# Kernel tuning notes

Hardware: AMD Instinct MI355X
Metric: run time of the kernel (lower is better)

The kernel has to match this reference:

```python
import jax, jax.numpy as jnp
import numpy as np

B, T, I, H, O = 64, 512, 256, 512, 256


def setup_inputs() -> dict:
    key = jax.random.key(0)
    ks = jax.random.split(key, 11)
    s_in = 1.0 / np.sqrt(H)  # torch nn.RNN init scale ~ U(-1/sqrt(H), 1/sqrt(H))
    return {
        "x": jax.random.normal(ks[0], (B, T, I), jnp.float32),
        "W_ih0": jax.random.normal(ks[1], (H, I), jnp.float32) * s_in,
        "W_hh0": jax.random.normal(ks[2], (H, H), jnp.float32) * s_in,
        "b_ih0": jax.random.normal(ks[3], (H,), jnp.float32) * s_in,
        "b_hh0": jax.random.normal(ks[4], (H,), jnp.float32) * s_in,
        "W_ih1": jax.random.normal(ks[5], (H, H), jnp.float32) * s_in,
        "W_hh1": jax.random.normal(ks[6], (H, H), jnp.float32) * s_in,
        "b_ih1": jax.random.normal(ks[7], (H,), jnp.float32) * s_in,
        "b_hh1": jax.random.normal(ks[8], (H,), jnp.float32) * s_in,
        "W_fc": jax.random.normal(ks[9], (O, H), jnp.float32) * s_in,
        "b_fc": jax.random.normal(ks[10], (O,), jnp.float32) * s_in,
    }


def _rnn_layer(xs, W_ih, W_hh, b_ih, b_hh):
    # xs: [T, B, in]; precompute input projection as one big GEMM
    pre = jnp.einsum("tbi,hi->tbh", xs, W_ih) + b_ih + b_hh  # [T, B, H]

    def step(h, p):
        h = jnp.tanh(p + h @ W_hh.T)
        return h, h

    h0 = jnp.zeros((xs.shape[1], W_hh.shape[0]), xs.dtype)
    h_last, ys = jax.lax.scan(step, h0, pre)
    return ys, h_last  # ys: [T, B, H]


def reference(x, W_ih0, W_hh0, b_ih0, b_hh0, W_ih1, W_hh1, b_ih1, b_hh1, W_fc, b_fc):
    xs = jnp.transpose(x, (1, 0, 2))  # time-major [T, B, I]
    ys0, _ = _rnn_layer(xs, W_ih0, W_hh0, b_ih0, b_hh0)
    _, h_last = _rnn_layer(ys0, W_ih1, W_hh1, b_ih1, b_hh1)
    return h_last @ W_fc.T + b_fc  # [B, O]
```

## Files before the change

kernel.cpp:

```cpp
#include <hip/hip_runtime.h>

#define BB 64
#define TT 512
#define II 256
#define HH 512
#define OO 256

typedef _Float16 f16;
typedef _Float16 half8 __attribute__((ext_vector_type(8)));
typedef _Float16 half4 __attribute__((ext_vector_type(4)));
typedef float f32x4 __attribute__((ext_vector_type(4)));
typedef unsigned long long u64;

#define SENT 0x7C017C017C017C01ull

union U16 { u64 q[2]; half8 h; };

__device__ __forceinline__ u64 llc_load(const f16* p) {
  return __hip_atomic_load((const u64*)p, __ATOMIC_RELAXED, __HIP_MEMORY_SCOPE_SYSTEM);
}
__device__ __forceinline__ void llc_store(f16* p, u64 v) {
  __hip_atomic_store((u64*)p, v, __ATOMIC_RELAXED, __HIP_MEMORY_SCOPE_SYSTEM);
}

__global__ void prep_sent(u64* __restrict__ dst, size_t n) {
  size_t tid = (size_t)blockIdx.x * blockDim.x + threadIdx.x;
  size_t stride = (size_t)gridDim.x * blockDim.x;
  for (size_t i = tid; i < n; i += stride) dst[i] = SENT;
}

__global__ void prep_x(const float* __restrict__ x, f16* __restrict__ xt) {
  size_t tid = (size_t)blockIdx.x * blockDim.x + threadIdx.x;
  size_t stride = (size_t)gridDim.x * blockDim.x;
  size_t nv = (size_t)TT * BB * II / 4;
  for (size_t v = tid; v < nv; v += stride) {
    size_t i = v * 4;
    size_t t = i >> 14;
    size_t rem = i & 16383;
    size_t b = rem >> 8;
    size_t ii = rem & 255;
    float4 f = *(const float4*)(x + b * (size_t)(TT * II) + t * II + ii);
    half4 h;
    h.x = (f16)f.x; h.y = (f16)f.y; h.z = (f16)f.z; h.w = (f16)f.w;
    *(half4*)(xt + i) = h;
  }
}

__global__ void prep_w(const float* __restrict__ wih0, const float* __restrict__ whh0,
                       const float* __restrict__ wih1, const float* __restrict__ whh1,
                       const float* __restrict__ bih0, const float* __restrict__ bhh0,
                       const float* __restrict__ bih1, const float* __restrict__ bhh1,
                       f16* __restrict__ o0, f16* __restrict__ o1,
                       f16* __restrict__ o2, f16* __restrict__ o3,
                       float* __restrict__ bs0, float* __restrict__ bs1) {
  const size_t n0 = (size_t)HH * II, n1 = (size_t)HH * HH;
  const size_t total = n0 + 3 * n1 + 2 * HH;
  size_t stride = (size_t)gridDim.x * blockDim.x;
  for (size_t i = (size_t)blockIdx.x * blockDim.x + threadIdx.x; i < total; i += stride) {
    size_t j = i;
    if (j < n0) { o0[j] = (f16)wih0[j]; continue; } j -= n0;
    if (j < n1) { o1[j] = (f16)whh0[j]; continue; } j -= n1;
    if (j < n1) { o2[j] = (f16)wih1[j]; continue; } j -= n1;
    if (j < n1) { o3[j] = (f16)whh1[j]; continue; } j -= n1;
    if (j < HH) { bs0[j] = bih0[j] + bhh0[j]; continue; } j -= HH;
    bs1[j] = bih1[j] + bhh1[j];
  }
}

__device__ __forceinline__ void load_valid16(const f16* base, u64* q) {
  for (int iter = 0; iter < 400000; ++iter) {
#pragma unroll
    for (int kf = 0; kf < 16; ++kf) {
      q[2 * kf]     = llc_load(base + kf * 32);
      q[2 * kf + 1] = llc_load(base + kf * 32 + 4);
    }
    int ok = 1;
#pragma unroll
    for (int i = 0; i < 32; ++i) ok &= (q[i] != SENT);
    if (__all(ok)) return;
  }
}

__global__ __launch_bounds__(64, 1) void rnn_seq(
    const f16* __restrict__ xt, f16* __restrict__ ys0, f16* __restrict__ h1h,
    const f16* __restrict__ wih0, const f16* __restrict__ whh0,
    const f16* __restrict__ wih1, const f16* __restrict__ whh1,
    const float* __restrict__ bs0, const float* __restrict__ bs1,
    const float* __restrict__ wfc, const float* __restrict__ bfc,
    float* __restrict__ out) {
  const int wg = blockIdx.x;
  const int layer = wg >> 6;
  const int c = (wg >> 4) & 3;
  const int s = wg & 15;
  const int lane = threadIdx.x;
  const int fr = lane & 15;
  const int kg = lane >> 4;
  const int n0 = s * 32;

  __shared__ f16 tile[16 * 32];

  if (layer == 0) {
    half8 wbi[2][8], wbh[2][16];
#pragma unroll
    for (int j = 0; j < 2; ++j) {
      const f16* wi = wih0 + (size_t)(n0 + j * 16 + fr) * II + kg * 8;
#pragma unroll
      for (int kf = 0; kf < 8; ++kf) wbi[j][kf] = *(const half8*)(wi + kf * 32);
      const f16* wh = whh0 + (size_t)(n0 + j * 16 + fr) * HH + kg * 8;
#pragma unroll
      for (int kf = 0; kf < 16; ++kf) wbh[j][kf] = *(const half8*)(wh + kf * 32);
    }
    const float bias[2] = {bs0[n0 + fr], bs0[n0 + 16 + fr]};
    f32x4 pacc[2][2] = {{{0,0,0,0},{0,0,0,0}},{{0,0,0,0},{0,0,0,0}}};
    {
      const f16* xa = xt + ((size_t)0 * BB + c * 16 + fr) * II + kg * 8;
#pragma unroll
      for (int kf = 0; kf < 8; ++kf) {
        half8 a = *(const half8*)(xa + kf * 32);
        pacc[0][kf & 1] = __builtin_amdgcn_mfma_f32_16x16x32_f16(a, wbi[0][kf], pacc[0][kf & 1], 0, 0, 0);
        pacc[1][kf & 1] = __builtin_amdgcn_mfma_f32_16x16x32_f16(a, wbi[1][kf], pacc[1][kf & 1], 0, 0, 0);
      }
    }
    for (int t = 0; t < TT; ++t) {
      f32x4 acc[2][2];
#pragma unroll
      for (int j = 0; j < 2; ++j) { acc[j][0] = pacc[j][0]; acc[j][1] = pacc[j][1]; }
      if (t > 0) {
        u64 q[32];
        load_valid16(ys0 + ((size_t)(t - 1) * BB + c * 16 + fr) * HH + kg * 8, q);
#pragma unroll
        for (int kf = 0; kf < 16; ++kf) {
          U16 u; u.q[0] = q[2 * kf]; u.q[1] = q[2 * kf + 1];
          acc[0][kf & 1] = __builtin_amdgcn_mfma_f32_16x16x32_f16(u.h, wbh[0][kf], acc[0][kf & 1], 0, 0, 0);
          acc[1][kf & 1] = __builtin_amdgcn_mfma_f32_16x16x32_f16(u.h, wbh[1][kf], acc[1][kf & 1], 0, 0, 0);
        }
      }
#pragma unroll
      for (int j = 0; j < 2; ++j)
#pragma unroll
        for (int r = 0; r < 4; ++r)
          tile[(kg * 4 + r) * 32 + j * 16 + fr] =
              (f16)tanhf(acc[j][0][r] + acc[j][1][r] + bias[j]);
      {
        U16 w; w.h = *(const half8*)(tile + lane * 8);
        f16* dst = ys0 + ((size_t)t * BB + c * 16 + (lane >> 2)) * HH + n0 + (lane & 3) * 8;
        llc_store(dst, w.q[0]);
        llc_store(dst + 4, w.q[1]);
      }
      if (t + 1 < TT) {
#pragma unroll
        for (int j = 0; j < 2; ++j) { pacc[j][0] = (f32x4){0,0,0,0}; pacc[j][1] = (f32x4){0,0,0,0}; }
        const f16* xa = xt + ((size_t)(t + 1) * BB + c * 16 + fr) * II + kg * 8;
#pragma unroll
        for (int kf = 0; kf < 8; ++kf) {
          half8 a = *(const half8*)(xa + kf * 32);
          pacc[0][kf & 1] = __builtin_amdgcn_mfma_f32_16x16x32_f16(a, wbi[0][kf], pacc[0][kf & 1], 0, 0, 0);
          pacc[1][kf & 1] = __builtin_amdgcn_mfma_f32_16x16x32_f16(a, wbi[1][kf], pacc[1][kf & 1], 0, 0, 0);
        }
      }
    }
  } else {
    half8 wbi[2][16], wbh[2][16];
#pragma unroll
    for (int j = 0; j < 2; ++j) {
      const f16* wi = wih1 + (size_t)(n0 + j * 16 + fr) * HH + kg * 8;
#pragma unroll
      for (int kf = 0; kf < 16; ++kf) wbi[j][kf] = *(const half8*)(wi + kf * 32);
      const f16* wh = whh1 + (size_t)(n0 + j * 16 + fr) * HH + kg * 8;
#pragma unroll
      for (int kf = 0; kf < 16; ++kf) wbh[j][kf] = *(const half8*)(wh + kf * 32);
    }
    const float bias[2] = {bs1[n0 + fr], bs1[n0 + 16 + fr]};
    for (int t = 0; t < TT; ++t) {
      f32x4 acc[2][2] = {{{0,0,0,0},{0,0,0,0}},{{0,0,0,0},{0,0,0,0}}};
      {
        u64 q[32];
        load_valid16(ys0 + ((size_t)t * BB + c * 16 + fr) * HH + kg * 8, q);
#pragma unroll
        for (int kf = 0; kf < 16; ++kf) {
          U16 u; u.q[0] = q[2 * kf]; u.q[1] = q[2 * kf + 1];
          acc[0][kf & 1] = __builtin_amdgcn_mfma_f32_16x16x32_f16(u.h, wbi[0][kf], acc[0][kf & 1], 0, 0, 0);
          acc[1][kf & 1] = __builtin_amdgcn_mfma_f32_16x16x32_f16(u.h, wbi[1][kf], acc[1][kf & 1], 0, 0, 0);
        }
      }
      if (t > 0) {
        u64 q[32];
        load_valid16(h1h + ((size_t)(t - 1) * BB + c * 16 + fr) * HH + kg * 8, q);
#pragma unroll
        for (int kf = 0; kf < 16; ++kf) {
          U16 u; u.q[0] = q[2 * kf]; u.q[1] = q[2 * kf + 1];
          acc[0][kf & 1] = __builtin_amdgcn_mfma_f32_16x16x32_f16(u.h, wbh[0][kf], acc[0][kf & 1], 0, 0, 0);
          acc[1][kf & 1] = __builtin_amdgcn_mfma_f32_16x16x32_f16(u.h, wbh[1][kf], acc[1][kf & 1], 0, 0, 0);
        }
      }
#pragma unroll
      for (int j = 0; j < 2; ++j)
#pragma unroll
        for (int r = 0; r < 4; ++r)
          tile[(kg * 4 + r) * 32 + j * 16 + fr] =
              (f16)tanhf(acc[j][0][r] + acc[j][1][r] + bias[j]);
      {
        U16 w; w.h = *(const half8*)(tile + lane * 8);
        f16* dst = h1h + ((size_t)t * BB + c * 16 + (lane >> 2)) * HH + n0 + (lane & 3) * 8;
        llc_store(dst, w.q[0]);
        llc_store(dst + 4, w.q[1]);
      }
    }
    {
      const int row = c * 16 + fr;
      const int col0 = s * 16 + kg * 4;
      const f16* hb = h1h + ((size_t)(TT - 1) * BB + row) * HH;
      float r0 = bfc[col0], r1 = bfc[col0 + 1], r2 = bfc[col0 + 2], r3 = bfc[col0 + 3];
      const float4* w0 = (const float4*)(wfc + (size_t)(col0 + 0) * HH);
      const float4* w1 = (const float4*)(wfc + (size_t)(col0 + 1) * HH);
      const float4* w2 = (const float4*)(wfc + (size_t)(col0 + 2) * HH);
      const float4* w3 = (const float4*)(wfc + (size_t)(col0 + 3) * HH);
      for (int ch = 0; ch < 8; ++ch) {
        u64 q[16];
        for (int iter = 0; iter < 400000; ++iter) {
#pragma unroll
          for (int i = 0; i < 16; ++i) q[i] = llc_load(hb + (ch * 16 + i) * 4);
          int ok = 1;
#pragma unroll
          for (int i = 0; i < 16; ++i) ok &= (q[i] != SENT);
          if (__all(ok)) break;
        }
#pragma unroll
        for (int i = 0; i < 16; ++i) {
          U16 u; u.q[0] = q[i]; u.q[1] = 0;
          int bi = ch * 16 + i;
          float h0 = (float)u.h[0], h1 = (float)u.h[1], h2 = (float)u.h[2], h3 = (float)u.h[3];
          float4 a = w0[bi], b = w1[bi], cc = w2[bi], d = w3[bi];
          r0 += h0 * a.x + h1 * a.y + h2 * a.z + h3 * a.w;
          r1 += h0 * b.x + h1 * b.y + h2 * b.z + h3 * b.w;
          r2 += h0 * cc.x + h1 * cc.y + h2 * cc.z + h3 * cc.w;
          r3 += h0 * d.x + h1 * d.y + h2 * d.z + h3 * d.w;
        }
      }
      float4 o = {r0, r1, r2, r3};
      *(float4*)(out + (size_t)row * OO + col0) = o;
    }
  }
}

extern "C" void kernel_launch(void* const* d_in, const int* in_sizes, int n_in,
                              void* d_out, int out_size, void* d_ws, size_t ws_size,
                              hipStream_t stream) {
  const float* x    = (const float*)d_in[0];
  const float* wih0 = (const float*)d_in[1];
  const float* whh0 = (const float*)d_in[2];
  const float* bih0 = (const float*)d_in[3];
  const float* bhh0 = (const float*)d_in[4];
  const float* wih1 = (const float*)d_in[5];
  const float* whh1 = (const float*)d_in[6];
  const float* bih1 = (const float*)d_in[7];
  const float* bhh1 = (const float*)d_in[8];
  const float* wfc  = (const float*)d_in[9];
  const float* bfc  = (const float*)d_in[10];
  float* out = (float*)d_out;

  char* base = (char*)d_ws;
  size_t off = 0;
  auto take = [&](size_t bytes) {
    char* r = base + off;
    off = (off + bytes + 255) & ~(size_t)255;
    return r;
  };
  f16* xt      = (f16*)take((size_t)TT * BB * II * 2);
  f16* ys0     = (f16*)take((size_t)TT * BB * HH * 2);
  f16* h1h     = (f16*)take((size_t)TT * BB * HH * 2);
  f16* fwih0   = (f16*)take((size_t)HH * II * 2);
  f16* fwhh0   = (f16*)take((size_t)HH * HH * 2);
  f16* fwih1   = (f16*)take((size_t)HH * HH * 2);
  f16* fwhh1   = (f16*)take((size_t)HH * HH * 2);
  float* bs0   = (float*)take(HH * 4);
  float* bs1   = (float*)take(HH * 4);
  (void)ws_size; (void)in_sizes; (void)n_in; (void)out_size;

  size_t n_u64 = (size_t)2 * TT * BB * HH / 4;
  prep_sent<<<dim3(2048), dim3(256), 0, stream>>>((u64*)ys0, n_u64);
  prep_x<<<dim3(1024), dim3(256), 0, stream>>>(x, xt);
  prep_w<<<dim3(512), dim3(256), 0, stream>>>(wih0, whh0, wih1, whh1,
                                              bih0, bhh0, bih1, bhh1,
                                              fwih0, fwhh0, fwih1, fwhh1, bs0, bs1);

  rnn_seq<<<dim3(128), dim3(64), 0, stream>>>(xt, ys0, h1h,
                                              fwih0, fwhh0, fwih1, fwhh1,
                                              bs0, bs1, wfc, bfc, out);
}
```

Baseline: 2.080 ms.

## Split RNN work across twice as many workgroups with LDS-resident weights and fast tanh

Doubles the persistent grid from 128 to 256 single-wave workgroups, so each one owns a 16-column slice of the hidden state instead of 32, halving the per-step MFMA work on the serial critical path. Weight fragments move from registers into LDS to fit the new layout. tanhf is replaced with an exp-based approximation. In layer 1 the loads of the previous hidden state are issued before the wait on the layer-0 input, so the two fetches overlap. In exchange there are more cross-workgroup sentinel polls and more LDS traffic, and the fast tanh may lose accuracy for inputs of large magnitude.

```diff
diff --git a/kernel.cpp b/kernel.cpp
--- a/kernel.cpp
+++ b/kernel.cpp
@@ -15,12 +15,17 @@
 #define SENT 0x7C017C017C017C01ull
 
 union U16 { u64 q[2]; half8 h; };
+union U8  { u64 q;    half4 h; };
 
 __device__ __forceinline__ u64 llc_load(const f16* p) {
   return __hip_atomic_load((const u64*)p, __ATOMIC_RELAXED, __HIP_MEMORY_SCOPE_SYSTEM);
 }
 __device__ __forceinline__ void llc_store(f16* p, u64 v) {
   __hip_atomic_store((u64*)p, v, __ATOMIC_RELAXED, __HIP_MEMORY_SCOPE_SYSTEM);
+}
+__device__ __forceinline__ float ftanh(float x) {
+  float e = __expf(2.0f * x);
+  return 1.0f - 2.0f / (e + 1.0f);
 }
 
 __global__ void prep_sent(u64* __restrict__ dst, size_t n) {
@@ -67,18 +72,25 @@
   }
 }
 
-__device__ __forceinline__ void load_valid16(const f16* base, u64* q) {
-  for (int iter = 0; iter < 400000; ++iter) {
-#pragma unroll
-    for (int kf = 0; kf < 16; ++kf) {
-      q[2 * kf]     = llc_load(base + kf * 32);
-      q[2 * kf + 1] = llc_load(base + kf * 32 + 4);
-    }
+__device__ __forceinline__ void issue32(const f16* base, u64* q) {
+#pragma unroll
+  for (int kf = 0; kf < 16; ++kf) {
+    q[2 * kf]     = llc_load(base + kf * 32);
+    q[2 * kf + 1] = llc_load(base + kf * 32 + 4);
+  }
+}
+__device__ __forceinline__ void validate32(const f16* base, u64* q) {
+  for (int it = 0; it < 200000; ++it) {
     int ok = 1;
 #pragma unroll
     for (int i = 0; i < 32; ++i) ok &= (q[i] != SENT);
     if (__all(ok)) return;
-  }
+    issue32(base, q);
+  }
+}
+__device__ __forceinline__ half8 frag(const u64* q, int kf) {
+  U16 u; u.q[0] = q[2 * kf]; u.q[1] = q[2 * kf + 1];
+  return u.h;
 }
 
 __global__ __launch_bounds__(64, 1) void rnn_seq(
@@ -89,135 +101,132 @@
     const float* __restrict__ wfc, const float* __restrict__ bfc,
     float* __restrict__ out) {
   const int wg = blockIdx.x;
-  const int layer = wg >> 6;
-  const int c = (wg >> 4) & 3;
-  const int s = wg & 15;
+  const int layer = wg >> 7;
+  const int c = (wg >> 5) & 3;
+  const int s = wg & 31;
   const int lane = threadIdx.x;
   const int fr = lane & 15;
   const int kg = lane >> 4;
-  const int n0 = s * 32;
-
-  __shared__ f16 tile[16 * 32];
+  const int n0 = s * 16;
+
+  __shared__ f16 wlds[32 * 64 * 8];
+  __shared__ f16 tile[16 * 16];
+
+  auto ldsw = [&](int slot) -> half8 {
+    return *(const half8*)(wlds + ((size_t)(slot * 64 + lane)) * 8);
+  };
 
   if (layer == 0) {
-    half8 wbi[2][8], wbh[2][16];
-#pragma unroll
-    for (int j = 0; j < 2; ++j) {
-      const f16* wi = wih0 + (size_t)(n0 + j * 16 + fr) * II + kg * 8;
-#pragma unroll
-      for (int kf = 0; kf < 8; ++kf) wbi[j][kf] = *(const half8*)(wi + kf * 32);
-      const f16* wh = whh0 + (size_t)(n0 + j * 16 + fr) * HH + kg * 8;
-#pragma unroll
-      for (int kf = 0; kf < 16; ++kf) wbh[j][kf] = *(const half8*)(wh + kf * 32);
-    }
-    const float bias[2] = {bs0[n0 + fr], bs0[n0 + 16 + fr]};
-    f32x4 pacc[2][2] = {{{0,0,0,0},{0,0,0,0}},{{0,0,0,0},{0,0,0,0}}};
+    {
+      const f16* wi = wih0 + (size_t)(n0 + fr) * II + kg * 8;
+#pragma unroll
+      for (int kf = 0; kf < 8; ++kf)
+        *(half8*)(wlds + (size_t)(kf * 64 + lane) * 8) = *(const half8*)(wi + kf * 32);
+      const f16* wh = whh0 + (size_t)(n0 + fr) * HH + kg * 8;
+#pragma unroll
+      for (int kf = 0; kf < 16; ++kf)
+        *(half8*)(wlds + (size_t)((8 + kf) * 64 + lane) * 8) = *(const half8*)(wh + kf * 32);
+    }
+    __syncthreads();
+    const float bias = bs0[n0 + fr];
+    f32x4 pA = {0,0,0,0}, pB = {0,0,0,0};
     {
       const f16* xa = xt + ((size_t)0 * BB + c * 16 + fr) * II + kg * 8;
 #pragma unroll
-      for (int kf = 0; kf < 8; ++kf) {
-        half8 a = *(const half8*)(xa + kf * 32);
-        pacc[0][kf & 1] = __builtin_amdgcn_mfma_f32_16x16x32_f16(a, wbi[0][kf], pacc[0][kf & 1], 0, 0, 0);
-        pacc[1][kf & 1] = __builtin_amdgcn_mfma_f32_16x16x32_f16(a, wbi[1][kf], pacc[1][kf & 1], 0, 0, 0);
+      for (int kf = 0; kf < 8; kf += 2) {
+        pA = __builtin_amdgcn_mfma_f32_16x16x32_f16(*(const half8*)(xa + kf * 32), ldsw(kf), pA, 0, 0, 0);
+        pB = __builtin_amdgcn_mfma_f32_16x16x32_f16(*(const half8*)(xa + (kf + 1) * 32), ldsw(kf + 1), pB, 0, 0, 0);
       }
     }
     for (int t = 0; t < TT; ++t) {
-      f32x4 acc[2][2];
-#pragma unroll
-      for (int j = 0; j < 2; ++j) { acc[j][0] = pacc[j][0]; acc[j][1] = pacc[j][1]; }
+      f32x4 aA = pA, aB = pB;
       if (t > 0) {
+        const f16* hb = ys0 + ((size_t)(t - 1) * BB + c * 16 + fr) * HH + kg * 8;
         u64 q[32];
-        load_valid16(ys0 + ((size_t)(t - 1) * BB + c * 16 + fr) * HH + kg * 8, q);
-#pragma unroll
-        for (int kf = 0; kf < 16; ++kf) {
-          U16 u; u.q[0] = q[2 * kf]; u.q[1] = q[2 * kf + 1];
-          acc[0][kf & 1] = __builtin_amdgcn_mfma_f32_16x16x32_f16(u.h, wbh[0][kf], acc[0][kf & 1], 0, 0, 0);
-          acc[1][kf & 1] = __builtin_amdgcn_mfma_f32_16x16x32_f16(u.h, wbh[1][kf], acc[1][kf & 1], 0, 0, 0);
-        }
-      }
-#pragma unroll
-      for (int j = 0; j < 2; ++j)
-#pragma unroll
-        for (int r = 0; r < 4; ++r)
-          tile[(kg * 4 + r) * 32 + j * 16 + fr] =
-              (f16)tanhf(acc[j][0][r] + acc[j][1][r] + bias[j]);
+        issue32(hb, q);
+        validate32(hb, q);
+#pragma unroll
+        for (int kf = 0; kf < 16; kf += 2) {
+          aA = __builtin_amdgcn_mfma_f32_16x16x32_f16(frag(q, kf), ldsw(8 + kf), aA, 0, 0, 0);
+          aB = __builtin_amdgcn_mfma_f32_16x16x32_f16(frag(q, kf + 1), ldsw(9 + kf), aB, 0, 0, 0);
+        }
+      }
+      f32x4 acc = aA + aB;
+      __syncthreads();
+#pragma unroll
+      for (int r = 0; r < 4; ++r)
+        tile[(kg * 4 + r) * 16 + fr] = (f16)ftanh(acc[r] + bias);
+      __syncthreads();
       {
-        U16 w; w.h = *(const half8*)(tile + lane * 8);
-        f16* dst = ys0 + ((size_t)t * BB + c * 16 + (lane >> 2)) * HH + n0 + (lane & 3) * 8;
-        llc_store(dst, w.q[0]);
-        llc_store(dst + 4, w.q[1]);
+        u64 w = *(const u64*)(tile + (lane >> 2) * 16 + (lane & 3) * 4);
+        llc_store(ys0 + ((size_t)t * BB + c * 16 + (lane >> 2)) * HH + n0 + (lane & 3) * 4, w);
       }
       if (t + 1 < TT) {
-#pragma unroll
-        for (int j = 0; j < 2; ++j) { pacc[j][0] = (f32x4){0,0,0,0}; pacc[j][1] = (f32x4){0,0,0,0}; }
+        pA = (f32x4){0,0,0,0}; pB = (f32x4){0,0,0,0};
         const f16* xa = xt + ((size_t)(t + 1) * BB + c * 16 + fr) * II + kg * 8;
 #pragma unroll
-        for (int kf = 0; kf < 8; ++kf) {
-          half8 a = *(const half8*)(xa + kf * 32);
-          pacc[0][kf & 1] = __builtin_amdgcn_mfma_f32_16x16x32_f16(a, wbi[0][kf], pacc[0][kf & 1], 0, 0, 0);
-          pacc[1][kf & 1] = __builtin_amdgcn_mfma_f32_16x16x32_f16(a, wbi[1][kf], pacc[1][kf & 1], 0, 0, 0);
+      for (int kf = 0; kf < 8; kf += 2) {
+          pA = __builtin_amdgcn_mfma_f32_16x16x32_f16(*(const half8*)(xa + kf * 32), ldsw(kf), pA, 0, 0, 0);
+          pB = __builtin_amdgcn_mfma_f32_16x16x32_f16(*(const half8*)(xa + (kf + 1) * 32), ldsw(kf + 1), pB, 0, 0, 0);
         }
       }
     }
   } else {
-    half8 wbi[2][16], wbh[2][16];
-#pragma unroll
-    for (int j = 0; j < 2; ++j) {
-      const f16* wi = wih1 + (size_t)(n0 + j * 16 + fr) * HH + kg * 8;
-#pragma unroll
-      for (int kf = 0; kf < 16; ++kf) wbi[j][kf] = *(const half8*)(wi + kf * 32);
-      const f16* wh = whh1 + (size_t)(n0 + j * 16 + fr) * HH + kg * 8;
-#pragma unroll
-      for (int kf = 0; kf < 16; ++kf) wbh[j][kf] = *(const half8*)(wh + kf * 32);
-    }
-    const float bias[2] = {bs1[n0 + fr], bs1[n0 + 16 + fr]};
+    {
+      const f16* wi = wih1 + (size_t)(n0 + fr) * HH + kg * 8;
+#pragma unroll
+      for (int kf = 0; kf < 16; ++kf)
+        *(half8*)(wlds + (size_t)(kf * 64 + lane) * 8) = *(const half8*)(wi + kf * 32);
+      const f16* wh = whh1 + (size_t)(n0 + fr) * HH + kg * 8;
+#pragma unroll
+      for (int kf = 0; kf < 16; ++kf)
+        *(half8*)(wlds + (size_t)((16 + kf) * 64 + lane) * 8) = *(const half8*)(wh + kf * 32);
+    }
+    __syncthreads();
+    const float bias = bs1[n0 + fr];
     for (int t = 0; t < TT; ++t) {
-      f32x4 acc[2][2] = {{{0,0,0,0},{0,0,0,0}},{{0,0,0,0},{0,0,0,0}}};
+      const f16* hb = h1h + ((size_t)(t - 1) * BB + c * 16 + fr) * HH + kg * 8;
+      u64 qh[32];
+      if (t > 0) issue32(hb, qh);
+      const f16* ib = ys0 + ((size_t)t * BB + c * 16 + fr) * HH + kg * 8;
+      u64 qi[32];
+      issue32(ib, qi);
+      validate32(ib, qi);
+      f32x4 aA = {0,0,0,0}, aB = {0,0,0,0};
+#pragma unroll
+      for (int kf = 0; kf < 16; kf += 2) {
+        aA = __builtin_amdgcn_mfma_f32_16x16x32_f16(frag(qi, kf), ldsw(kf), aA, 0, 0, 0);
+        aB = __builtin_amdgcn_mfma_f32_16x16x32_f16(frag(qi, kf + 1), ldsw(kf + 1), aB, 0, 0, 0);
+      }
+      if (t > 0) {
+        validate32(hb, qh);
+#pragma unroll
+        for (int kf = 0; kf < 16; kf += 2) {
+          aA = __builtin_amdgcn_mfma_f32_16x16x32_f16(frag(qh, kf), ldsw(16 + kf), aA, 0, 0, 0);
+          aB = __builtin_amdgcn_mfma_f32_16x16x32_f16(frag(qh, kf + 1), ldsw(17 + kf), aB, 0, 0, 0);
+        }
+      }
+      f32x4 acc = aA + aB;
+      __syncthreads();
+#pragma unroll
+      for (int r = 0; r < 4; ++r)
+        tile[(kg * 4 + r) * 16 + fr] = (f16)ftanh(acc[r] + bias);
+      __syncthreads();
       {
-        u64 q[32];
-        load_valid16(ys0 + ((size_t)t * BB + c * 16 + fr) * HH + kg * 8, q);
-#pragma unroll
-        for (int kf = 0; kf < 16; ++kf) {
-          U16 u; u.q[0] = q[2 * kf]; u.q[1] = q[2 * kf + 1];
-          acc[0][kf & 1] = __builtin_amdgcn_mfma_f32_16x16x32_f16(u.h, wbi[0][kf], acc[0][kf & 1], 0, 0, 0);
-          acc[1][kf & 1] = __builtin_amdgcn_mfma_f32_16x16x32_f16(u.h, wbi[1][kf], acc[1][kf & 1], 0, 0, 0);
-        }
-      }
-      if (t > 0) {
-        u64 q[32];
-        load_valid16(h1h + ((size_t)(t - 1) * BB + c * 16 + fr) * HH + kg * 8, q);
-#pragma unroll
-        for (int kf = 0; kf < 16; ++kf) {
-          U16 u; u.q[0] = q[2 * kf]; u.q[1] = q[2 * kf + 1];
-          acc[0][kf & 1] = __builtin_amdgcn_mfma_f32_16x16x32_f16(u.h, wbh[0][kf], acc[0][kf & 1], 0, 0, 0);
-          acc[1][kf & 1] = __builtin_amdgcn_mfma_f32_16x16x32_f16(u.h, wbh[1][kf], acc[1][kf & 1], 0, 0, 0);
-        }
-      }
-#pragma unroll
-      for (int j = 0; j < 2; ++j)
-#pragma unroll
-        for (int r = 0; r < 4; ++r)
-          tile[(kg * 4 + r) * 32 + j * 16 + fr] =
-              (f16)tanhf(acc[j][0][r] + acc[j][1][r] + bias[j]);
-      {
-        U16 w; w.h = *(const half8*)(tile + lane * 8);
-        f16* dst = h1h + ((size_t)t * BB + c * 16 + (lane >> 2)) * HH + n0 + (lane & 3) * 8;
-        llc_store(dst, w.q[0]);
-        llc_store(dst + 4, w.q[1]);
+        u64 w = *(const u64*)(tile + (lane >> 2) * 16 + (lane & 3) * 4);
+        llc_store(h1h + ((size_t)t * BB + c * 16 + (lane >> 2)) * HH + n0 + (lane & 3) * 4, w);
       }
     }
     {
       const int row = c * 16 + fr;
-      const int col0 = s * 16 + kg * 4;
+      const int col0 = s * 8 + kg * 2;
       const f16* hb = h1h + ((size_t)(TT - 1) * BB + row) * HH;
-      float r0 = bfc[col0], r1 = bfc[col0 + 1], r2 = bfc[col0 + 2], r3 = bfc[col0 + 3];
+      float r0 = bfc[col0], r1 = bfc[col0 + 1];
       const float4* w0 = (const float4*)(wfc + (size_t)(col0 + 0) * HH);
       const float4* w1 = (const float4*)(wfc + (size_t)(col0 + 1) * HH);
-      const float4* w2 = (const float4*)(wfc + (size_t)(col0 + 2) * HH);
-      const float4* w3 = (const float4*)(wfc + (size_t)(col0 + 3) * HH);
       for (int ch = 0; ch < 8; ++ch) {
         u64 q[16];
-        for (int iter = 0; iter < 400000; ++iter) {
+        for (int iter = 0; iter < 200000; ++iter) {
 #pragma unroll
           for (int i = 0; i < 16; ++i) q[i] = llc_load(hb + (ch * 16 + i) * 4);
           int ok = 1;
@@ -227,18 +236,16 @@
         }
 #pragma unroll
         for (int i = 0; i < 16; ++i) {
-          U16 u; u.q[0] = q[i]; u.q[1] = 0;
+          U8 u; u.q = q[i];
           int bi = ch * 16 + i;
-          float h0 = (float)u.h[0], h1 = (float)u.h[1], h2 = (float)u.h[2], h3 = (float)u.h[3];
-          float4 a = w0[bi], b = w1[bi], cc = w2[bi], d = w3[bi];
+          float h0 = (float)u.h.x, h1 = (float)u.h.y, h2 = (float)u.h.z, h3 = (float)u.h.w;
+          float4 a = w0[bi], b = w1[bi];
           r0 += h0 * a.x + h1 * a.y + h2 * a.z + h3 * a.w;
           r1 += h0 * b.x + h1 * b.y + h2 * b.z + h3 * b.w;
-          r2 += h0 * cc.x + h1 * cc.y + h2 * cc.z + h3 * cc.w;
-          r3 += h0 * d.x + h1 * d.y + h2 * d.z + h3 * d.w;
-        }
-      }
-      float4 o = {r0, r1, r2, r3};
-      *(float4*)(out + (size_t)row * OO + col0) = o;
+        }
+      }
+      out[(size_t)row * OO + col0] = r0;
+      out[(size_t)row * OO + col0 + 1] = r1;
     }
   }
 }
@@ -284,7 +291,7 @@
                                               bih0, bhh0, bih1, bhh1,
                                               fwih0, fwhh0, fwih1, fwhh1, bs0, bs1);
 
-  rnn_seq<<<dim3(128), dim3(64), 0, stream>>>(xt, ys0, h1h,
+  rnn_seq<<<dim3(256), dim3(64), 0, stream>>>(xt, ys0, h1h,
                                               fwih0, fwhh0, fwih1, fwhh1,
                                               bs0, bs1, wfc, bfc, out);
 }
```

Result: slower. 2.833 ms (+36.2%).
